# Kernel optimization log

Measured on AMD Instinct MI355X. Metric: run time of the kernel, lower is better.

## Reference

```python
import jax, jax.numpy as jnp
import numpy as np

T, N, M = 16, 10000, 2048          # timesteps, total nodes, masked nodes per step
F_IN, F1, F2, H = 256, 256, 256, 256  # feats_per_node, layer_1, layer_2, lstm_feats


def setup_inputs() -> dict:
    key = jax.random.key(0)
    ks = jax.random.split(key, 9)
    A = jax.random.normal(ks[0], (T, M, M), jnp.float32) / np.float32(np.sqrt(M))
    node_feats = jax.random.normal(ks[1], (N, F_IN), jnp.float32)
    # unique sorted indices per timestep (scatter target must be duplicate-free)
    mask = jax.vmap(lambda k: jnp.sort(jax.random.permutation(k, N)[:M]))(
        jax.random.split(ks[2], T)).astype(jnp.int32)
    u = lambda k, sh, fan: jax.random.uniform(k, sh, jnp.float32, -1.0, 1.0) * (2.0 / np.sqrt(fan))
    w0 = u(ks[3], (F_IN, F1), F_IN)
    w1 = u(ks[4], (F1, F2), F1)
    s = 1.0 / np.sqrt(H)
    W_ih = jax.random.uniform(ks[5], (4 * H, F2), jnp.float32, -s, s)
    W_hh = jax.random.uniform(ks[6], (4 * H, H), jnp.float32, -s, s)
    b_ih = jax.random.uniform(ks[7], (4 * H,), jnp.float32, -s, s)
    b_hh = jax.random.uniform(ks[8], (4 * H,), jnp.float32, -s, s)
    return {"A": A, "node_feats": node_feats, "mask": mask, "w0": w0, "w1": w1,
            "W_ih": W_ih, "W_hh": W_hh, "b_ih": b_ih, "b_hh": b_hh}


def reference(A, node_feats, mask, w0, w1, W_ih, W_hh, b_ih, b_hh):
    def gcn_step(Ah, idx):
        # layer 0: x = X @ W0 ; x[idx] = act(Ahat @ x[idx])
        x = node_feats @ w0                               # [N, F1]
        x = x.at[idx].set(jax.nn.relu(Ah @ x[idx]))
        # layer 1
        x = x @ w1                                        # [N, F2]
        x = x.at[idx].set(jax.nn.relu(Ah @ x[idx]))
        return x

    seq = jax.vmap(gcn_step)(A, mask)                     # [T, N, F2]

    def lstm_step(carry, xt):
        h, c = carry
        z = xt @ W_ih.T + h @ W_hh.T + (b_ih + b_hh)      # [N, 4H]
        i, f, g, o = jnp.split(z, 4, axis=-1)             # torch gate order i,f,g,o
        c = jax.nn.sigmoid(f) * c + jax.nn.sigmoid(i) * jnp.tanh(g)
        h = jax.nn.sigmoid(o) * jnp.tanh(c)
        return (h, c), None

    h0 = jnp.zeros((N, H), seq.dtype)
    (h, _), _ = jax.lax.scan(lstm_step, (h0, h0), seq)
    return h                                              # out[-1] of single-layer LSTM
```

## Files before the change

kernel.cpp:

```cpp
#include <hip/hip_runtime.h>
#include <cstdint>
#include <cstddef>

#pragma clang diagnostic ignored "-Waddress-space-conversion"

constexpr int T  = 16;
constexpr int N  = 10000;
constexpr int M  = 2048;
constexpr int F  = 256;
constexpr int H  = 256;
constexpr int G4 = 1024;
constexpr int NP = 10112;

typedef _Float16 f16;
using half8  = __attribute__((ext_vector_type(8))) f16;
using half4  = __attribute__((ext_vector_type(4))) f16;
using half2v = __attribute__((ext_vector_type(2))) f16;
using f32x4  = __attribute__((ext_vector_type(4))) float;

typedef __attribute__((address_space(1))) const void gas_t;
typedef __attribute__((address_space(3))) void las_t;

__device__ __forceinline__ void gl_lds16(const f16* g, f16* l) {
    __builtin_amdgcn_global_load_lds((gas_t*)g, (las_t*)l, 16, 0, 0);
}

template<bool AF32, bool RELU, int OMODE>
__global__ __launch_bounds__(256, 2)
void gemm16(const void* __restrict__ Ag, long long sA,
            const f16*  __restrict__ Bg, long long sB,
            void*       __restrict__ Cg, long long sC,
            int Kk, int Nn, int Mvalid, int ldct)
{
    __shared__ f16 Als[2][128 * 32];
    __shared__ f16 Bls[2][128 * 32];

    const int tid  = threadIdx.x;
    const int lane = tid & 63;
    const int w    = tid >> 6;
    const int wm   = w >> 1, wn = w & 1;
    const int m0   = blockIdx.y * 128, n0 = blockIdx.x * 128;
    const int z    = blockIdx.z;

    const f16* Bt = Bg + (size_t)z * sB;
    const int srow = lane >> 2;
    const int scol = (lane & 3) * 8;

    f32x4 acc[4][4] = {};

    auto stage = [&](int buf, int kt) {
        const int k0 = kt * 32;
        #pragma unroll
        for (int c = 0; c < 2; ++c) {
            const int brow = w * 32 + c * 16;
            gl_lds16(Bt + (size_t)(n0 + brow + srow) * Kk + k0 + scol,
                     &Bls[buf][brow * 32]);
        }
        if constexpr (AF32) {
            const float* Af = (const float*)Ag + (size_t)z * sA;
            #pragma unroll
            for (int p = 0; p < 4; ++p) {
                const int flat = p * 1024 + tid * 4;
                const int r = flat >> 5, cc = flat & 31;
                float4 v = *(const float4*)&Af[(size_t)(m0 + r) * Kk + k0 + cc];
                half4 hv = { (f16)v.x, (f16)v.y, (f16)v.z, (f16)v.w };
                *(half4*)&Als[buf][r * 32 + cc] = hv;
            }
        } else {
            const f16* Af = (const f16*)Ag + (size_t)z * sA;
            #pragma unroll
            for (int c = 0; c < 2; ++c) {
                const int arow = w * 32 + c * 16;
                gl_lds16(Af + (size_t)(m0 + arow + srow) * Kk + k0 + scol,
                         &Als[buf][arow * 32]);
            }
        }
    };

    const int nk = Kk >> 5;
    stage(0, 0);
    int cur = 0;
    const int fr = lane & 15, fg = lane >> 4;

    for (int kt = 0; kt < nk; ++kt) {
        __syncthreads();
        if (kt + 1 < nk) stage(cur ^ 1, kt + 1);

        half8 a[4], b[4];
        #pragma unroll
        for (int i = 0; i < 4; ++i)
            a[i] = *(const half8*)&Als[cur][(wm * 64 + i * 16 + fr) * 32 + fg * 8];
        #pragma unroll
        for (int j = 0; j < 4; ++j)
            b[j] = *(const half8*)&Bls[cur][(wn * 64 + j * 16 + fr) * 32 + fg * 8];
        #pragma unroll
        for (int i = 0; i < 4; ++i)
            #pragma unroll
            for (int j = 0; j < 4; ++j)
                acc[i][j] = __builtin_amdgcn_mfma_f32_16x16x32_f16(a[i], b[j], acc[i][j], 0, 0, 0);
        cur ^= 1;
    }

    #pragma unroll
    for (int i = 0; i < 4; ++i) {
        const int gmb = m0 + wm * 64 + i * 16 + fg * 4;
        #pragma unroll
        for (int j = 0; j < 4; ++j) {
            const int gn = n0 + wn * 64 + j * 16 + fr;
            f32x4 v = acc[i][j];
            if (RELU) {
                v[0] = fmaxf(v[0], 0.f); v[1] = fmaxf(v[1], 0.f);
                v[2] = fmaxf(v[2], 0.f); v[3] = fmaxf(v[3], 0.f);
            }
            if constexpr (OMODE == 1) {
                f16* Ch = (f16*)Cg + (size_t)z * sC;
                #pragma unroll
                for (int r = 0; r < 4; ++r)
                    if (gmb + r < Mvalid) Ch[(size_t)(gmb + r) * Nn + gn] = (f16)v[r];
            } else {
                f16* Ct = (f16*)Cg + (size_t)z * sC;
                half4 hv = { (f16)v[0], (f16)v[1], (f16)v[2], (f16)v[3] };
                if (gmb + 3 < Mvalid) *(half4*)&Ct[(size_t)gn * ldct + gmb] = hv;
            }
        }
    }
}

__global__ __launch_bounds__(256, 2)
void gemm_lstm(const f16* __restrict__ h16, const f16* __restrict__ Whh,
               const f16* __restrict__ U, const f16* __restrict__ V,
               const int* __restrict__ invt, const float* __restrict__ bsum,
               float* __restrict__ Cb, f16* __restrict__ h16_out,
               float* __restrict__ hout)
{
    __shared__ f16 Als[2][128 * 32];
    __shared__ f16 Bls[2][128 * 32];

    const int tid  = threadIdx.x;
    const int lane = tid & 63;
    const int w    = tid >> 6;
    const int wm   = w >> 1, wn = w & 1;
    const int m0   = blockIdx.y * 128, n0 = blockIdx.x * 128;

    const int srow = lane >> 2;
    const int scol = (lane & 3) * 8;

    f32x4 acc[4][4] = {};

    auto stage = [&](int buf, int kt) {
        const int k0 = kt * 32;
        #pragma unroll
        for (int c = 0; c < 2; ++c) {
            const int row = w * 32 + c * 16;
            gl_lds16(Whh + (size_t)(n0 + row + srow) * H + k0 + scol, &Bls[buf][row * 32]);
            gl_lds16(h16 + (size_t)(m0 + row + srow) * H + k0 + scol, &Als[buf][row * 32]);
        }
    };

    stage(0, 0);
    int cur = 0;
    const int fr = lane & 15, fg = lane >> 4;

    for (int kt = 0; kt < H / 32; ++kt) {
        __syncthreads();
        if (kt + 1 < H / 32) stage(cur ^ 1, kt + 1);
        half8 a[4], b[4];
        #pragma unroll
        for (int i = 0; i < 4; ++i)
            a[i] = *(const half8*)&Als[cur][(wm * 64 + i * 16 + fr) * 32 + fg * 8];
        #pragma unroll
        for (int j = 0; j < 4; ++j)
            b[j] = *(const half8*)&Bls[cur][(wn * 64 + j * 16 + fr) * 32 + fg * 8];
        #pragma unroll
        for (int i = 0; i < 4; ++i)
            #pragma unroll
            for (int j = 0; j < 4; ++j)
                acc[i][j] = __builtin_amdgcn_mfma_f32_16x16x32_f16(a[i], b[j], acc[i][j], 0, 0, 0);
        cur ^= 1;
    }

    const int u = ((n0 >> 6) + wn) * 16 + fr;
    const int colbase = n0 + wn * 64 + fr;
    const float b0 = bsum[colbase], b1 = bsum[colbase + 16],
                b2 = bsum[colbase + 32], b3 = bsum[colbase + 48];
    auto sig = [](float x) { return 1.f / (1.f + __expf(-x)); };

    #pragma unroll
    for (int i = 0; i < 4; ++i) {
        const int nodeb = m0 + wm * 64 + i * 16 + fg * 4;
        #pragma unroll
        for (int r = 0; r < 4; ++r) {
            const int node = nodeb + r;
            if (node >= N) continue;
            const int p = invt[node];
            const f16* xb = (p >= 0) ? V + (size_t)p * G4 : U + (size_t)node * G4;
            const float zi = acc[i][0][r] + (float)xb[colbase]      + b0;
            const float zf = acc[i][1][r] + (float)xb[colbase + 16] + b1;
            const float zg = acc[i][2][r] + (float)xb[colbase + 32] + b2;
            const float zo = acc[i][3][r] + (float)xb[colbase + 48] + b3;
            const size_t ci = (size_t)node * H + u;
            const float c = sig(zf) * Cb[ci] + sig(zi) * tanhf(zg);
            Cb[ci] = c;
            const float hv = sig(zo) * tanhf(c);
            h16_out[ci] = (f16)hv;
            if (hout) hout[ci] = hv;
        }
    }
}

__global__ __launch_bounds__(256)
void gather_T(const f16* __restrict__ Y0h, const int* __restrict__ mask,
              f16* __restrict__ GT)
{
    __shared__ f16 tile[64][F + 8];
    const int t = blockIdx.y, p0 = blockIdx.x * 64;
    const int tid = threadIdx.x;
    const int pr = tid >> 2;
    const int fc = (tid & 3) * 8;

    const int row = mask[t * M + p0 + pr];
    const f16* src = Y0h + (size_t)row * F;
    #pragma unroll
    for (int it = 0; it < 8; ++it) {
        const int f = it * 32 + fc;
        *(half8*)&tile[pr][f] = *(const half8*)&src[f];
    }
    __syncthreads();

    f16* dst = GT + ((size_t)t * F + tid) * M + p0;
    #pragma unroll
    for (int pc = 0; pc < 64; pc += 8) {
        half8 v;
        #pragma unroll
        for (int r = 0; r < 8; ++r) v[r] = tile[pc + r][tid];
        *(half8*)&dst[pc] = v;
    }
}

__global__ void cvt_f16(const float* __restrict__ s, f16* __restrict__ d, long long n)
{
    long long base = ((long long)blockIdx.x * blockDim.x + threadIdx.x) * 4;
    if (base + 3 < n) {
        float4 v = *(const float4*)&s[base];
        half4 hv = { (f16)v.x, (f16)v.y, (f16)v.z, (f16)v.w };
        *(half4*)&d[base] = hv;
    } else {
        for (long long k = base; k < n; ++k) d[k] = (f16)s[k];
    }
}

__global__ void cvtT_f16(const float* __restrict__ s, f16* __restrict__ d, int R, int C)
{
    int i = blockIdx.x * 256 + threadIdx.x;
    if (i >= R * C) return;
    int r = i % R, c = i / R;
    d[(size_t)c * R + r] = (f16)s[(size_t)r * C + c];
}

__global__ void permW(const float* __restrict__ s, f16* __restrict__ d, int K)
{
    const int pcol = blockIdx.x;
    const int c64 = pcol >> 6, within = pcol & 63, gate = within >> 4, r = within & 15;
    const int srow = gate * 256 + c64 * 16 + r;
    const float* sp = s + (size_t)srow * K;
    f16* dp = d + (size_t)pcol * K;
    const int k = threadIdx.x * 4;
    float4 v = *(const float4*)&sp[k];
    half4 hv = { (f16)v.x, (f16)v.y, (f16)v.z, (f16)v.w };
    *(half4*)&dp[k] = hv;
}

__global__ void bias_perm(const float* __restrict__ bi, const float* __restrict__ bh,
                          float* __restrict__ bsum)
{
    const int pcol = blockIdx.x * 256 + threadIdx.x;
    if (pcol >= G4) return;
    const int c64 = pcol >> 6, within = pcol & 63, gate = within >> 4, r = within & 15;
    const int srow = gate * 256 + c64 * 16 + r;
    bsum[pcol] = bi[srow] + bh[srow];
}

__global__ void build_inv(const int* __restrict__ mask, int* __restrict__ inv)
{
    int i = blockIdx.x * blockDim.x + threadIdx.x;
    if (i >= T * M) return;
    int t = i / M;
    inv[(size_t)t * N + mask[i]] = i % M;
}

extern "C" void kernel_launch(void* const* d_in, const int* in_sizes, int n_in,
                              void* d_out, int out_size, void* d_ws, size_t ws_size,
                              hipStream_t stream)
{
    const float* A_all = (const float*)d_in[0];
    const float* nf    = (const float*)d_in[1];
    const int*   mask  = (const int*)  d_in[2];
    const float* w0    = (const float*)d_in[3];
    const float* w1    = (const float*)d_in[4];
    const float* W_ih  = (const float*)d_in[5];
    const float* W_hh  = (const float*)d_in[6];
    const float* b_ih  = (const float*)d_in[7];
    const float* b_hh  = (const float*)d_in[8];
    float* h = (float*)d_out;

    char* wp = (char*)d_ws;
    auto alloc = [&](size_t bytes) { char* p = wp; wp += (bytes + 255) & ~(size_t)255; return p; };
    f16*   nf16  = (f16*)alloc((size_t)NP * F * 2);
    f16*   w0T   = (f16*)alloc((size_t)F * F * 2);
    f16*   w1T   = (f16*)alloc((size_t)F * F * 2);
    f16*   Wih16 = (f16*)alloc((size_t)G4 * F * 2);
    f16*   Whh16 = (f16*)alloc((size_t)G4 * H * 2);
    float* bsum  = (float*)alloc((size_t)G4 * 4);
    f16*   Y0h   = (f16*)alloc((size_t)NP * F * 2);
    f16*   Y1h   = (f16*)alloc((size_t)NP * F * 2);
    f16*   Uh    = (f16*)alloc((size_t)NP * G4 * 2);
    f16*   GT    = (f16*)alloc((size_t)T * F * M * 2);
    f16*   Z1b   = (f16*)alloc((size_t)T * M * F * 2);
    f16*   Z2T   = (f16*)alloc((size_t)T * F * M * 2);
    f16*   Z3b   = (f16*)alloc((size_t)T * M * F * 2);
    f16*   Vb    = (f16*)alloc((size_t)4 * M * G4 * 2);
    float* Cb    = (float*)alloc((size_t)N * H * 4);
    f16*   h16   = (f16*)alloc((size_t)NP * H * 2);
    int*   inv   = (int*)alloc((size_t)T * N * 4);

    hipMemsetAsync(Cb,  0,    (size_t)N * H * 4,  stream);
    hipMemsetAsync(h16, 0,    (size_t)NP * H * 2, stream);
    hipMemsetAsync(nf16,0,    (size_t)NP * F * 2, stream);
    hipMemsetAsync(inv, 0xFF, (size_t)T * N * 4,  stream);

    build_inv<<<(T * M + 255) / 256, 256, 0, stream>>>(mask, inv);
    cvt_f16 <<<((long long)N * F / 4 + 255) / 256, 256, 0, stream>>>(nf, nf16, (long long)N * F);
    cvtT_f16<<<(F * F + 255) / 256, 256, 0, stream>>>(w0, w0T, F, F);
    cvtT_f16<<<(F * F + 255) / 256, 256, 0, stream>>>(w1, w1T, F, F);
    permW<<<G4, 64, 0, stream>>>(W_ih, Wih16, F);
    permW<<<G4, 64, 0, stream>>>(W_hh, Whh16, H);
    bias_perm<<<(G4 + 255) / 256, 256, 0, stream>>>(b_ih, b_hh, bsum);

    gemm16<false,false,1><<<dim3(F / 128,  NP / 128, 1), 256, 0, stream>>>(nf16, 0, w0T,   0, Y0h, 0, F, F,  NP, 0);
    gemm16<false,false,1><<<dim3(F / 128,  NP / 128, 1), 256, 0, stream>>>(Y0h,  0, w1T,   0, Y1h, 0, F, F,  NP, 0);
    gemm16<false,false,1><<<dim3(G4 / 128, NP / 128, 1), 256, 0, stream>>>(Y1h,  0, Wih16, 0, Uh,  0, F, G4, NP, 0);

    gather_T<<<dim3(M / 64, T), 256, 0, stream>>>(Y0h, mask, GT);

    const long long sAmm = (long long)M * M;
    const long long sFM  = (long long)F * M;
    const long long sMF  = (long long)M * F;
    gemm16<true, true, 1><<<dim3(2, 16, T), 256, 0, stream>>>(A_all, sAmm, GT,  sFM, Z1b, sMF, M, F, M, 0);
    gemm16<false,false,2><<<dim3(2, 16, T), 256, 0, stream>>>(Z1b,  sMF,  w1T, 0,   Z2T, sFM, F, F, M, M);
    gemm16<true, true, 1><<<dim3(2, 16, T), 256, 0, stream>>>(A_all, sAmm, Z2T, sFM, Z3b, sMF, M, F, M, 0);

    for (int t = 0; t < T; ++t) {
        if ((t & 3) == 0) {
            gemm16<false,false,1><<<dim3(G4 / 128, M / 128, 4), 256, 0, stream>>>(
                Z3b + (size_t)t * M * F, sMF, Wih16, 0, Vb, (long long)M * G4, F, G4, M, 0);
        }
        gemm_lstm<<<dim3(G4 / 128, NP / 128, 1), 256, 0, stream>>>(
            h16, Whh16, Uh, Vb + (size_t)(t & 3) * M * G4, inv + (size_t)t * N,
            bsum, Cb, h16, (t == T - 1) ? h : nullptr);
    }
}
```

Baseline: 792.7 us.

## Add wide-N fp32-A GEMM, fold LSTM bias into input GEMMs, store cell state in fp16

Result: slower. 836.6 us (+5.5%).

```diff
diff --git a/kernel.cpp b/kernel.cpp
--- a/kernel.cpp
+++ b/kernel.cpp
@@ -15,7 +15,6 @@
 typedef _Float16 f16;
 using half8  = __attribute__((ext_vector_type(8))) f16;
 using half4  = __attribute__((ext_vector_type(4))) f16;
-using half2v = __attribute__((ext_vector_type(2))) f16;
 using f32x4  = __attribute__((ext_vector_type(4))) float;
 
 typedef __attribute__((address_space(1))) const void gas_t;
@@ -25,12 +24,13 @@
     __builtin_amdgcn_global_load_lds((gas_t*)g, (las_t*)l, 16, 0, 0);
 }
 
-template<bool AF32, bool RELU, int OMODE>
+template<bool RELU, int OMODE>
 __global__ __launch_bounds__(256, 2)
-void gemm16(const void* __restrict__ Ag, long long sA,
-            const f16*  __restrict__ Bg, long long sB,
-            void*       __restrict__ Cg, long long sC,
-            int Kk, int Nn, int Mvalid, int ldct)
+void gemm16(const f16* __restrict__ Ag, long long sA,
+            const f16* __restrict__ Bg, long long sB,
+            void*      __restrict__ Cg, long long sC,
+            int Kk, int Nn, int Mvalid, int ldct,
+            const float* __restrict__ bias)
 {
     __shared__ f16 Als[2][128 * 32];
     __shared__ f16 Bls[2][128 * 32];
@@ -42,6 +42,7 @@
     const int m0   = blockIdx.y * 128, n0 = blockIdx.x * 128;
     const int z    = blockIdx.z;
 
+    const f16* At = Ag + (size_t)z * sA;
     const f16* Bt = Bg + (size_t)z * sB;
     const int srow = lane >> 2;
     const int scol = (lane & 3) * 8;
@@ -52,28 +53,9 @@
         const int k0 = kt * 32;
         #pragma unroll
         for (int c = 0; c < 2; ++c) {
-            const int brow = w * 32 + c * 16;
-            gl_lds16(Bt + (size_t)(n0 + brow + srow) * Kk + k0 + scol,
-                     &Bls[buf][brow * 32]);
-        }
-        if constexpr (AF32) {
-            const float* Af = (const float*)Ag + (size_t)z * sA;
-            #pragma unroll
-            for (int p = 0; p < 4; ++p) {
-                const int flat = p * 1024 + tid * 4;
-                const int r = flat >> 5, cc = flat & 31;
-                float4 v = *(const float4*)&Af[(size_t)(m0 + r) * Kk + k0 + cc];
-                half4 hv = { (f16)v.x, (f16)v.y, (f16)v.z, (f16)v.w };
-                *(half4*)&Als[buf][r * 32 + cc] = hv;
-            }
-        } else {
-            const f16* Af = (const f16*)Ag + (size_t)z * sA;
-            #pragma unroll
-            for (int c = 0; c < 2; ++c) {
-                const int arow = w * 32 + c * 16;
-                gl_lds16(Af + (size_t)(m0 + arow + srow) * Kk + k0 + scol,
-                         &Als[buf][arow * 32]);
-            }
+            const int row = w * 32 + c * 16;
+            gl_lds16(Bt + (size_t)(n0 + row + srow) * Kk + k0 + scol, &Bls[buf][row * 32]);
+            gl_lds16(At + (size_t)(m0 + row + srow) * Kk + k0 + scol, &Als[buf][row * 32]);
         }
     };
 
@@ -102,15 +84,17 @@
     }
 
     #pragma unroll
-    for (int i = 0; i < 4; ++i) {
-        const int gmb = m0 + wm * 64 + i * 16 + fg * 4;
-        #pragma unroll
-        for (int j = 0; j < 4; ++j) {
-            const int gn = n0 + wn * 64 + j * 16 + fr;
+    for (int j = 0; j < 4; ++j) {
+        const int gn = n0 + wn * 64 + j * 16 + fr;
+        const float bb = bias ? bias[gn] : 0.f;
+        #pragma unroll
+        for (int i = 0; i < 4; ++i) {
+            const int gmb = m0 + wm * 64 + i * 16 + fg * 4;
             f32x4 v = acc[i][j];
-            if (RELU) {
-                v[0] = fmaxf(v[0], 0.f); v[1] = fmaxf(v[1], 0.f);
-                v[2] = fmaxf(v[2], 0.f); v[3] = fmaxf(v[3], 0.f);
+            #pragma unroll
+            for (int r = 0; r < 4; ++r) {
+                v[r] += bb;
+                if (RELU) v[r] = fmaxf(v[r], 0.f);
             }
             if constexpr (OMODE == 1) {
                 f16* Ch = (f16*)Cg + (size_t)z * sC;
@@ -126,11 +110,89 @@
     }
 }
 
+__global__ __launch_bounds__(512, 1)
+void gemmA(const float* __restrict__ Ag, long long sA,
+           const f16*  __restrict__ Bg, long long sB,
+           f16*        __restrict__ Cg, long long sC)
+{
+    __shared__ f16 Als[2][128 * 32];
+    __shared__ f16 Bls[2][256 * 32];
+
+    const int tid  = threadIdx.x;
+    const int lane = tid & 63;
+    const int w    = tid >> 6;
+    const int wm   = w >> 2, wn = w & 3;
+    const int m0   = blockIdx.x * 128;
+    const int z    = blockIdx.y;
+
+    const float* A = Ag + (size_t)z * sA;
+    const f16*   B = Bg + (size_t)z * sB;
+    f16*         C = Cg + (size_t)z * sC;
+
+    const int srow = lane >> 2;
+    const int scol = (lane & 3) * 8;
+
+    f32x4 acc[4][4] = {};
+
+    auto stage = [&](int buf, int kt) {
+        const int k0 = kt * 32;
+        #pragma unroll
+        for (int c = 0; c < 2; ++c) {
+            const int row = w * 32 + c * 16;
+            gl_lds16(B + (size_t)(row + srow) * M + k0 + scol, &Bls[buf][row * 32]);
+        }
+        #pragma unroll
+        for (int p = 0; p < 2; ++p) {
+            const int flat = p * 2048 + tid * 4;
+            const int r = flat >> 5, cc = flat & 31;
+            float4 v = *(const float4*)&A[(size_t)(m0 + r) * M + k0 + cc];
+            half4 hv = { (f16)v.x, (f16)v.y, (f16)v.z, (f16)v.w };
+            *(half4*)&Als[buf][r * 32 + cc] = hv;
+        }
+    };
+
+    stage(0, 0);
+    int cur = 0;
+    const int fr = lane & 15, fg = lane >> 4;
+
+    for (int kt = 0; kt < M / 32; ++kt) {
+        __syncthreads();
+        if (kt + 1 < M / 32) stage(cur ^ 1, kt + 1);
+
+        half8 a[4], b[4];
+        #pragma unroll
+        for (int i = 0; i < 4; ++i)
+            a[i] = *(const half8*)&Als[cur][(wm * 64 + i * 16 + fr) * 32 + fg * 8];
+        #pragma unroll
+        for (int j = 0; j < 4; ++j)
+            b[j] = *(const half8*)&Bls[cur][(wn * 64 + j * 16 + fr) * 32 + fg * 8];
+        #pragma unroll
+        for (int i = 0; i < 4; ++i)
+            #pragma unroll
+            for (int j = 0; j < 4; ++j)
+                acc[i][j] = __builtin_amdgcn_mfma_f32_16x16x32_f16(a[i], b[j], acc[i][j], 0, 0, 0);
+        cur ^= 1;
+    }
+
+    #pragma unroll
+    for (int i = 0; i < 4; ++i) {
+        const int gmb = m0 + wm * 64 + i * 16 + fg * 4;
+        #pragma unroll
+        for (int j = 0; j < 4; ++j) {
+            const int gn = wn * 64 + j * 16 + fr;
+            f32x4 v = acc[i][j];
+            #pragma unroll
+            for (int r = 0; r < 4; ++r)
+                C[(size_t)(gmb + r) * F + gn] = (f16)fmaxf(v[r], 0.f);
+        }
+    }
+}
+
 __global__ __launch_bounds__(256, 2)
 void gemm_lstm(const f16* __restrict__ h16, const f16* __restrict__ Whh,
                const f16* __restrict__ U, const f16* __restrict__ V,
-               const int* __restrict__ invt, const float* __restrict__ bsum,
-               float* __restrict__ Cb, f16* __restrict__ h16_out,
+               const int* __restrict__ invt,
+               f16* __restrict__ Cb, f16* __restrict__ h16_out,
                float* __restrict__ hout)
 {
     __shared__ f16 Als[2][128 * 32];
@@ -181,8 +243,6 @@
 
     const int u = ((n0 >> 6) + wn) * 16 + fr;
     const int colbase = n0 + wn * 64 + fr;
-    const float b0 = bsum[colbase], b1 = bsum[colbase + 16],
-                b2 = bsum[colbase + 32], b3 = bsum[colbase + 48];
     auto sig = [](float x) { return 1.f / (1.f + __expf(-x)); };
 
     #pragma unroll
@@ -194,13 +254,13 @@
             if (node >= N) continue;
             const int p = invt[node];
             const f16* xb = (p >= 0) ? V + (size_t)p * G4 : U + (size_t)node * G4;
-            const float zi = acc[i][0][r] + (float)xb[colbase]      + b0;
-            const float zf = acc[i][1][r] + (float)xb[colbase + 16] + b1;
-            const float zg = acc[i][2][r] + (float)xb[colbase + 32] + b2;
-            const float zo = acc[i][3][r] + (float)xb[colbase + 48] + b3;
+            const float zi = acc[i][0][r] + (float)xb[colbase];
+            const float zf = acc[i][1][r] + (float)xb[colbase + 16];
+            const float zg = acc[i][2][r] + (float)xb[colbase + 32];
+            const float zo = acc[i][3][r] + (float)xb[colbase + 48];
             const size_t ci = (size_t)node * H + u;
-            const float c = sig(zf) * Cb[ci] + sig(zi) * tanhf(zg);
-            Cb[ci] = c;
+            const float c = sig(zf) * (float)Cb[ci] + sig(zi) * tanhf(zg);
+            Cb[ci] = (f16)c;
             const float hv = sig(zo) * tanhf(c);
             h16_out[ci] = (f16)hv;
             if (hout) hout[ci] = hv;
@@ -319,11 +379,11 @@
     f16*   Z2T   = (f16*)alloc((size_t)T * F * M * 2);
     f16*   Z3b   = (f16*)alloc((size_t)T * M * F * 2);
     f16*   Vb    = (f16*)alloc((size_t)4 * M * G4 * 2);
-    float* Cb    = (float*)alloc((size_t)N * H * 4);
+    f16*   Cb    = (f16*)alloc((size_t)N * H * 2);
     f16*   h16   = (f16*)alloc((size_t)NP * H * 2);
     int*   inv   = (int*)alloc((size_t)T * N * 4);
 
-    hipMemsetAsync(Cb,  0,    (size_t)N * H * 4,  stream);
+    hipMemsetAsync(Cb,  0,    (size_t)N * H * 2,  stream);
     hipMemsetAsync(h16, 0,    (size_t)NP * H * 2, stream);
     hipMemsetAsync(nf16,0,    (size_t)NP * F * 2, stream);
     hipMemsetAsync(inv, 0xFF, (size_t)T * N * 4,  stream);
@@ -336,26 +396,26 @@
     permW<<<G4, 64, 0, stream>>>(W_hh, Whh16, H);
     bias_perm<<<(G4 + 255) / 256, 256, 0, stream>>>(b_ih, b_hh, bsum);
 
-    gemm16<false,false,1><<<dim3(F / 128,  NP / 128, 1), 256, 0, stream>>>(nf16, 0, w0T,   0, Y0h, 0, F, F,  NP, 0);
-    gemm16<false,false,1><<<dim3(F / 128,  NP / 128, 1), 256, 0, stream>>>(Y0h,  0, w1T,   0, Y1h, 0, F, F,  NP, 0);
-    gemm16<false,false,1><<<dim3(G4 / 128, NP / 128, 1), 256, 0, stream>>>(Y1h,  0, Wih16, 0, Uh,  0, F, G4, NP, 0);
+    gemm16<false,1><<<dim3(F / 128,  NP / 128, 1), 256, 0, stream>>>(nf16, 0, w0T,   0, Y0h, 0, F, F,  NP, 0, nullptr);
+    gemm16<false,1><<<dim3(F / 128,  NP / 128, 1), 256, 0, stream>>>(Y0h,  0, w1T,   0, Y1h, 0, F, F,  NP, 0, nullptr);
+    gemm16<false,1><<<dim3(G4 / 128, NP / 128, 1), 256, 0, stream>>>(Y1h,  0, Wih16, 0, Uh,  0, F, G4, NP, 0, bsum);
 
     gather_T<<<dim3(M / 64, T), 256, 0, stream>>>(Y0h, mask, GT);
 
     const long long sAmm = (long long)M * M;
     const long long sFM  = (long long)F * M;
     const long long sMF  = (long long)M * F;
-    gemm16<true, true, 1><<<dim3(2, 16, T), 256, 0, stream>>>(A_all, sAmm, GT,  sFM, Z1b, sMF, M, F, M, 0);
-    gemm16<false,false,2><<<dim3(2, 16, T), 256, 0, stream>>>(Z1b,  sMF,  w1T, 0,   Z2T, sFM, F, F, M, M);
-    gemm16<true, true, 1><<<dim3(2, 16, T), 256, 0, stream>>>(A_all, sAmm, Z2T, sFM, Z3b, sMF, M, F, M, 0);
+    gemmA<<<dim3(M / 128, T), 512, 0, stream>>>(A_all, sAmm, GT, sFM, Z1b, sMF);
+    gemm16<false,2><<<dim3(2, 16, T), 256, 0, stream>>>(Z1b, sMF, w1T, 0, Z2T, sFM, F, F, M, M, nullptr);
+    gemmA<<<dim3(M / 128, T), 512, 0, stream>>>(A_all, sAmm, Z2T, sFM, Z3b, sMF);
 
     for (int t = 0; t < T; ++t) {
         if ((t & 3) == 0) {
-            gemm16<false,false,1><<<dim3(G4 / 128, M / 128, 4), 256, 0, stream>>>(
-                Z3b + (size_t)t * M * F, sMF, Wih16, 0, Vb, (long long)M * G4, F, G4, M, 0);
+            gemm16<false,1><<<dim3(G4 / 128, M / 128, 4), 256, 0, stream>>>(
+                Z3b + (size_t)t * M * F, sMF, Wih16, 0, Vb, (long long)M * G4, F, G4, M, 0, bsum);
         }
         gemm_lstm<<<dim3(G4 / 128, NP / 128, 1), 256, 0, stream>>>(
             h16, Whh16, Uh, Vb + (size_t)(t & 3) * M * G4, inv + (size_t)t * N,
-            bsum, Cb, h16, (t == T - 1) ? h : nullptr);
-    }
-}
+            Cb, h16, (t == T - 1) ? h : nullptr);
+    }
+}
```
